# Performance work log

Measured on AMD Instinct MI355X. Metric: run time of the kernel, lower is better.

Reference implementation:

```python
import jax, jax.numpy as jnp
import numpy as np

NUM_HEADS = 8
CH_PER_HEAD = 40
NORM_GROUPS = 32
EPS = 1e-5


def setup_inputs() -> dict:
    key = jax.random.key(0)
    ks = jax.random.split(key, 8)
    B, C, H, W = 2, 320, 48, 48
    hid = NUM_HEADS * CH_PER_HEAD  # 320
    w_std = 0.02
    return {
        "x": jax.random.normal(ks[0], (B, C, H, W), dtype=jnp.float32),
        "gamma": jnp.ones((C,), dtype=jnp.float32),
        "beta": jnp.zeros((C,), dtype=jnp.float32),
        "Wq": jax.random.normal(ks[1], (hid, C), dtype=jnp.float32) * w_std,
        "bq": jax.random.normal(ks[2], (hid,), dtype=jnp.float32) * w_std,
        "Wk": jax.random.normal(ks[3], (hid, C), dtype=jnp.float32) * w_std,
        "bk": jax.random.normal(ks[4], (hid,), dtype=jnp.float32) * w_std,
        "Wv": jax.random.normal(ks[5], (hid, C), dtype=jnp.float32) * w_std,
        "bv": jax.random.normal(ks[6], (hid,), dtype=jnp.float32) * w_std,
        "Wo": jax.random.normal(ks[7], (C, hid), dtype=jnp.float32) * w_std,
        "bo": jnp.zeros((C,), dtype=jnp.float32),
    }


def _group_norm(x, gamma, beta):
    # x: [B, C, H, W]; GroupNorm over (C//G, H, W) per group, affine per-channel.
    B, C, H, W = x.shape
    xg = x.reshape(B, NORM_GROUPS, C // NORM_GROUPS, H, W)
    mean = xg.mean(axis=(2, 3, 4), keepdims=True)
    var = xg.var(axis=(2, 3, 4), keepdims=True)
    xn = ((xg - mean) * jax.lax.rsqrt(var + EPS)).reshape(B, C, H, W)
    return xn * gamma[None, :, None, None] + beta[None, :, None, None]


def reference(x, gamma, beta, Wq, bq, Wk, bk, Wv, bv, Wo, bo):
    B, C, H, W = x.shape
    N = H * W
    h, d = NUM_HEADS, CH_PER_HEAD
    scale = d ** (-0.25)  # applied to both q and k (net 1/sqrt(d))

    xn = _group_norm(x, gamma, beta).reshape(B, C, N)  # embedding = x_n (self-attn)

    # 1x1 Conv1d == matmul over channel dim
    q = jnp.einsum('oc,bcn->bon', Wq, xn) + bq[None, :, None]
    k = jnp.einsum('oc,bcn->bon', Wk, xn) + bk[None, :, None]
    v = jnp.einsum('oc,bcn->bon', Wv, xn) + bv[None, :, None]

    # b (h d) n -> b h d n
    q = q.reshape(B, h, d, N)
    k = k.reshape(B, h, d, N)
    v = v.reshape(B, h, d, N)

    attn = jax.nn.softmax(
        jnp.einsum('bhdi,bhdj->bhij', q * scale, k * scale), axis=-1
    )  # [B, h, N, N]
    out = jnp.einsum('bhij,bhdj->bhdi', attn, v).reshape(B, h * d, N)

    out = jnp.einsum('oc,bcn->bon', Wo, out) + bo[None, :, None]
    out = out.reshape(B, C, H, W)
    return x + out  # shapes match -> residual
```

## Files before the change

kernel.cpp:

```cpp
#include <hip/hip_runtime.h>
#include <hip/hip_bf16.h>

#define C_DIM   320
#define N_SP    2304
#define NHEADS  8
#define DHEAD   40
#define GROUPS  32
#define CPG     10
#define BATCH   2
#define DPAD    64
#define VPAD    48
#define W_ELEMS (C_DIM * C_DIM)
#define NSPLIT  4
#define TILES_PER_SPLIT 9
#define PSLOTS  41

typedef __bf16 bf16x8 __attribute__((ext_vector_type(8)));
typedef __bf16 bf16x4 __attribute__((ext_vector_type(4)));
typedef __bf16 bf16x2 __attribute__((ext_vector_type(2)));
typedef float  f32x4  __attribute__((ext_vector_type(4)));

typedef const __attribute__((address_space(1))) void* gas_ptr;
typedef __attribute__((address_space(3))) void* las_ptr;

#define MFMA16(a, b, c) __builtin_amdgcn_mfma_f32_16x16x32_bf16((a), (b), (c), 0, 0, 0)

__device__ __forceinline__ void stage8(const char* gbase, char* lbase,
                                       int chunk, int lane)
{
    const int row = chunk * 8 + (lane >> 3);
    const int cs  = (lane & 7) * 16;
    __builtin_amdgcn_global_load_lds(
        (gas_ptr)(gbase + (size_t)row * (C_DIM * 2) + (cs ^ ((row & 7) << 4))),
        (las_ptr)(lbase + chunk * 1024 + lane * 16), 16, 0, 0);
}

__device__ __forceinline__ bf16x8 lds_frag(const char* lbase, int row, int cbyte)
{
    return *(const bf16x8*)(lbase + row * 128 + (cbyte ^ ((row & 7) << 4)));
}

__global__ __launch_bounds__(256) void prep_kernel(
    const float* __restrict__ x, float* __restrict__ partials,
    const float* __restrict__ Wq, const float* __restrict__ Wk,
    const float* __restrict__ Wv, const float* __restrict__ Wo,
    __bf16* __restrict__ Wqb, __bf16* __restrict__ Wkb,
    __bf16* __restrict__ Wvb, __bf16* __restrict__ Wob,
    __bf16* __restrict__ Qt, __bf16* __restrict__ Kt, __bf16* __restrict__ Vb)
{
    if (blockIdx.x < 512) {
        const int bid = blockIdx.x;
        const int bg = bid >> 3, p = bid & 7;
        const int b = bg >> 5, g = bg & 31;
        const float* xp = x + ((size_t)b * C_DIM + g * CPG) * N_SP + p * 288;
        const int tid = threadIdx.x;

        float sum = 0.f, sq = 0.f;
        #pragma unroll
        for (int c = 0; c < CPG; ++c) {
            for (int nl = tid; nl < 288; nl += 256) {
                const float v = xp[(size_t)c * N_SP + nl];
                sum += v; sq += v * v;
            }
        }
        #pragma unroll
        for (int off = 32; off; off >>= 1) {
            sum += __shfl_xor(sum, off);
            sq  += __shfl_xor(sq, off);
        }
        __shared__ float red[2][4];
        if ((tid & 63) == 0) { red[0][tid >> 6] = sum; red[1][tid >> 6] = sq; }
        __syncthreads();
        if (tid == 0) {
            partials[2 * bid]     = red[0][0] + red[0][1] + red[0][2] + red[0][3];
            partials[2 * bid + 1] = red[1][0] + red[1][1] + red[1][2] + red[1][3];
        }
    } else if (blockIdx.x < 612) {
        const int i = ((blockIdx.x - 512) * 256 + threadIdx.x) * 4;
        f32x4 a;
        bf16x4 o;
        a = *(const f32x4*)(Wq + i);
        #pragma unroll
        for (int e = 0; e < 4; ++e) o[e] = (__bf16)a[e];
        *(bf16x4*)(Wqb + i) = o;
        a = *(const f32x4*)(Wk + i);
        #pragma unroll
        for (int e = 0; e < 4; ++e) o[e] = (__bf16)a[e];
        *(bf16x4*)(Wkb + i) = o;
        a = *(const f32x4*)(Wv + i);
        #pragma unroll
        for (int e = 0; e < 4; ++e) o[e] = (__bf16)a[e];
        *(bf16x4*)(Wvb + i) = o;
        a = *(const f32x4*)(Wo + i);
        #pragma unroll
        for (int e = 0; e < 4; ++e) o[e] = (__bf16)a[e];
        *(bf16x4*)(Wob + i) = o;
    } else {
        const int t = (blockIdx.x - 612) * 256 + threadIdx.x;
        const bf16x8 z = {};
        __bf16* q = Qt + (size_t)t * DPAD + 40;
        __bf16* k = Kt + (size_t)t * DPAD + 40;
        *(bf16x8*)(q) = z; *(bf16x8*)(q + 8) = z; *(bf16x8*)(q + 16) = z;
        *(bf16x8*)(k) = z; *(bf16x8*)(k + 8) = z; *(bf16x8*)(k + 16) = z;
        const int bh = t / N_SP;
        const int rem = t - bh * N_SP;
        const int r = rem / 288, n8 = rem - r * 288;
        bf16x8 v = z;
        if (r == 0) {
            #pragma unroll
            for (int e = 0; e < 8; ++e) v[e] = (__bf16)1.0f;
        }
        *(bf16x8*)(Vb + ((size_t)bh * VPAD + 40 + r) * N_SP + n8 * 8) = v;
    }
}

__global__ __launch_bounds__(256) void gn_apply(
    const float* __restrict__ x,
    const float* __restrict__ gamma, const float* __restrict__ beta,
    const float* __restrict__ partials, __bf16* __restrict__ xn_t)
{
    const int bid = blockIdx.x;
    const int bg = bid >> 3, p = bid & 7;
    const int b = bg >> 5, g = bg & 31;
    const int c0 = g * CPG;

    float sum = 0.f, sq = 0.f;
    #pragma unroll
    for (int i = 0; i < 8; ++i) {
        sum += partials[(bg * 8 + i) * 2];
        sq  += partials[(bg * 8 + i) * 2 + 1];
    }
    const float inv_n = 1.0f / (float)(CPG * N_SP);
    const float mean = sum * inv_n;
    const float rstd = rsqrtf(sq * inv_n - mean * mean + 1e-5f);

    float ga[CPG], be[CPG];
    #pragma unroll
    for (int c = 0; c < CPG; ++c) {
        ga[c] = gamma[c0 + c] * rstd;
        be[c] = beta[c0 + c] - mean * ga[c];
    }

    const float* xp = x + ((size_t)b * C_DIM + c0) * N_SP + p * 288;
    for (int nl = threadIdx.x; nl < 288; nl += 256) {
        const int n = p * 288 + nl;
        __bf16* dst = xn_t + ((size_t)b * N_SP + n) * C_DIM + c0;
        #pragma unroll
        for (int j = 0; j < CPG / 2; ++j) {
            const float v0 = xp[(size_t)(2 * j) * N_SP + nl]     * ga[2 * j]     + be[2 * j];
            const float v1 = xp[(size_t)(2 * j + 1) * N_SP + nl] * ga[2 * j + 1] + be[2 * j + 1];
            bf16x2 t; t[0] = (__bf16)v0; t[1] = (__bf16)v1;
            *(bf16x2*)(dst + 2 * j) = t;
        }
    }
}

__global__ __launch_bounds__(256) void gemm_qkv(
    const __bf16* __restrict__ Wqb, const __bf16* __restrict__ Wkb, const __bf16* __restrict__ Wvb,
    const float* __restrict__ bq, const float* __restrict__ bk, const float* __restrict__ bv,
    const __bf16* __restrict__ Xt,
    __bf16* __restrict__ Qt, __bf16* __restrict__ Kt, __bf16* __restrict__ Vb)
{
    __shared__ __align__(16) char Ws[2][64 * 128];
    __shared__ __align__(16) char Xs[2][64 * 128];

    const int z = blockIdx.z;
    const int b = z / 3;
    const int which = z - 3 * b;
    const __bf16* W   = (which == 0) ? Wqb : (which == 1) ? Wkb : Wvb;
    const float* bias = (which == 0) ? bq : (which == 1) ? bk : bv;
    const float scale = (which == 0) ? 0.15811388300841897f
                      : (which == 1) ? 0.22811243f : 1.0f;

    const int n0 = blockIdx.x * 64, o0 = blockIdx.y * 64;
    const int tid = threadIdx.x, wave = tid >> 6, lane = tid & 63;
    const int lr = lane & 15, lk = lane >> 4;
    const int wm = wave >> 1, wn = wave & 1;

    const char* Wg = (const char*)(W + (size_t)o0 * C_DIM);
    const char* Xg = (const char*)(Xt + ((size_t)b * N_SP + n0) * C_DIM);

    auto stage = [&](int bufi, int s) {
        const int kb = s * 128;
        #pragma unroll
        for (int i = 0; i < 4; ++i) {
            const int c = wave * 4 + i;
            if (c < 8) stage8(Wg + kb, Ws[bufi], c, lane);
            else       stage8(Xg + kb, Xs[bufi], c - 8, lane);
        }
    };

    f32x4 acc[2][2] = {};

    stage(0, 0);
    __syncthreads();

    for (int s = 0; s < 5; ++s) {
        const int bufi = s & 1;
        if (s + 1 < 5) stage(bufi ^ 1, s + 1);

        const char* ws = Ws[bufi];
        const char* xs = Xs[bufi];
        __builtin_amdgcn_s_setprio(1);
        #pragma unroll
        for (int ksub = 0; ksub < 2; ++ksub) {
            const int cb = ksub * 64 + lk * 16;
            const bf16x8 a0 = lds_frag(ws, wm * 32 + lr,      cb);
            const bf16x8 a1 = lds_frag(ws, wm * 32 + 16 + lr, cb);
            const bf16x8 b0 = lds_frag(xs, wn * 32 + lr,      cb);
            const bf16x8 b1 = lds_frag(xs, wn * 32 + 16 + lr, cb);
            acc[0][0] = MFMA16(a0, b0, acc[0][0]);
            acc[0][1] = MFMA16(a0, b1, acc[0][1]);
            acc[1][0] = MFMA16(a1, b0, acc[1][0]);
            acc[1][1] = MFMA16(a1, b1, acc[1][1]);
        }
        __builtin_amdgcn_s_setprio(0);
        __syncthreads();
    }

    #pragma unroll
    for (int am = 0; am < 2; ++am) {
        #pragma unroll
        for (int rp = 0; rp < 2; ++rp) {
            const int o = o0 + wm * 32 + am * 16 + 4 * lk + 2 * rp;
            const int h = o / DHEAD, d = o - h * DHEAD;
            const int bh = b * NHEADS + h;
            const float b0_ = bias[o], b1_ = bias[o + 1];
            #pragma unroll
            for (int bn = 0; bn < 2; ++bn) {
                const int n = n0 + wn * 32 + bn * 16 + lr;
                const float v0 = (acc[am][bn][2 * rp]     + b0_) * scale;
                const float v1 = (acc[am][bn][2 * rp + 1] + b1_) * scale;
                if (which < 2) {
                    __bf16* dst = ((which == 0) ? Qt : Kt)
                                + ((size_t)bh * N_SP + n) * DPAD + d;
                    bf16x2 t; t[0] = (__bf16)v0; t[1] = (__bf16)v1;
                    *(bf16x2*)dst = t;
                } else {
                    Vb[((size_t)bh * VPAD + d)     * N_SP + n] = (__bf16)v0;
                    Vb[((size_t)bh * VPAD + d + 1) * N_SP + n] = (__bf16)v1;
                }
            }
        }
    }
}

__global__ __launch_bounds__(256) void gemm_out32(
    const __bf16* __restrict__ Wob, const float* __restrict__ bo,
    const __bf16* __restrict__ att_t,
    float* __restrict__ Y, const float* __restrict__ resid)
{
    __shared__ __align__(16) char Ws[2][32 * 128];
    __shared__ __align__(16) char Xs[2][64 * 128];

    const int b = blockIdx.z;
    const int n0 = blockIdx.x * 64, o0 = blockIdx.y * 32;
    const int tid = threadIdx.x, wave = tid >> 6, lane = tid & 63;
    const int lr = lane & 15, lk = lane >> 4;
    const int wn = wave;

    const char* Wg = (const char*)(Wob + (size_t)o0 * C_DIM);
    const char* Xg = (const char*)(att_t + ((size_t)b * N_SP + n0) * C_DIM);

    auto stage = [&](int bufi, int s) {
        const int kb = s * 128;
        #pragma unroll
        for (int i = 0; i < 3; ++i) {
            const int c = wave * 3 + i;
            if (c < 4) stage8(Wg + kb, Ws[bufi], c, lane);
            else       stage8(Xg + kb, Xs[bufi], c - 4, lane);
        }
    };

    f32x4 acc[2] = {};

    stage(0, 0);
    __syncthreads();

    for (int s = 0; s < 5; ++s) {
        const int bufi = s & 1;
        if (s + 1 < 5) stage(bufi ^ 1, s + 1);

        const char* ws = Ws[bufi];
        const char* xs = Xs[bufi];
        __builtin_amdgcn_s_setprio(1);
        #pragma unroll
        for (int ksub = 0; ksub < 2; ++ksub) {
            const int cb = ksub * 64 + lk * 16;
            const bf16x8 a0 = lds_frag(ws, lr,      cb);
            const bf16x8 a1 = lds_frag(ws, 16 + lr, cb);
            const bf16x8 b0 = lds_frag(xs, wn * 16 + lr, cb);
            acc[0] = MFMA16(a0, b0, acc[0]);
            acc[1] = MFMA16(a1, b0, acc[1]);
        }
        __builtin_amdgcn_s_setprio(0);
        __syncthreads();
    }

    const int n = n0 + wn * 16 + lr;
    #pragma unroll
    for (int am = 0; am < 2; ++am) {
        #pragma unroll
        for (int r = 0; r < 4; ++r) {
            const int o = o0 + am * 16 + 4 * lk + r;
            const size_t idx = ((size_t)b * C_DIM + o) * N_SP + n;
            Y[idx] = acc[am][r] + bo[o] + resid[idx];
        }
    }
}

__global__ __launch_bounds__(256) void attn_mfma(
    const __bf16* __restrict__ Qt,
    const __bf16* __restrict__ Kt,
    const __bf16* __restrict__ Vb,
    __bf16* __restrict__ part)
{
    __shared__ __align__(16) __bf16 Ks[2][64 * DPAD];
    __shared__ __align__(16) __bf16 Vs[2][VPAD * 64];
    __shared__ __align__(16) __bf16 Ps[4][16 * 64];

    const int flat = blockIdx.x;
    const int bh = ((flat & 7) << 1) | ((flat >> 3) & 1);
    const int s  = (flat >> 4) & 3;
    const int qx = flat >> 6;
    const int tid = threadIdx.x, wave = tid >> 6, lane = tid & 63;
    const int lr = lane & 15, lk = lane >> 4;
    const int swz = (lr & 7) << 4;
    const int i0 = (qx * 4 + wave) * 16;

    const char* Kg = (const char*)(Kt + (size_t)bh * N_SP * DPAD);
    const char* Vg = (const char*)(Vb + (size_t)bh * VPAD * N_SP);

    const __bf16* Qp = Qt + ((size_t)bh * N_SP + i0 + lr) * DPAD + lk * 8;
    const bf16x8 qb0 = *(const bf16x8*)(Qp);
    const bf16x8 qb1 = *(const bf16x8*)(Qp + 32);

    f32x4 O[3] = {};

    auto stage = [&](int bufi, int t) {
        const int j0 = t * 64;
        #pragma unroll
        for (int i2 = 0; i2 < 2; ++i2) {
            const int chunk = wave * 2 + i2;
            const int L = chunk * 1024 + lane * 16;
            const int src = L ^ (((L >> 7) & 7) << 4);
            __builtin_amdgcn_global_load_lds(
                (gas_ptr)(Kg + (size_t)j0 * 128 + src),
                (las_ptr)((char*)Ks[bufi] + chunk * 1024),
                16, 0, 0);
        }
        for (int i2 = wave; i2 < 6; i2 += 4) {
            const int row = i2 * 8 + (lane >> 3);
            const int csw = ((lane & 7) << 4) ^ ((row & 7) << 4);
            __builtin_amdgcn_global_load_lds(
                (gas_ptr)(Vg + ((size_t)row * N_SP + j0) * 2 + csw),
                (las_ptr)((char*)Vs[bufi] + i2 * 1024),
                16, 0, 0);
        }
    };

    const int t0 = s * TILES_PER_SPLIT;
    const int t1 = t0 + TILES_PER_SPLIT;

    stage(0, t0);

    for (int t = t0; t < t1; ++t) {
        const int bufi = (t - t0) & 1;
        if (t + 1 < t1) {
            stage(bufi ^ 1, t + 1);
            if (wave < 2) asm volatile("s_waitcnt vmcnt(4)" ::: "memory");
            else          asm volatile("s_waitcnt vmcnt(3)" ::: "memory");
        } else {
            asm volatile("s_waitcnt vmcnt(0)" ::: "memory");
        }
        __builtin_amdgcn_s_barrier();

        const char* ks = (const char*)Ks[bufi];
        const char* vs = (const char*)Vs[bufi];
        char* ps = (char*)Ps[wave];

        f32x4 S[4];
        __builtin_amdgcn_s_setprio(1);
        #pragma unroll
        for (int kt = 0; kt < 4; ++kt) {
            const int rowb = (kt * 16 + lr) * 128;
            const bf16x8 k0 = *(const bf16x8*)(ks + rowb + ((lk * 16) ^ swz));
            const bf16x8 k1 = *(const bf16x8*)(ks + rowb + ((64 + lk * 16) ^ swz));
            f32x4 zz = {};
            zz = MFMA16(k0, qb0, zz);
            S[kt] = MFMA16(k1, qb1, zz);
        }
        __builtin_amdgcn_s_setprio(0);

        #pragma unroll
        for (int kt = 0; kt < 4; ++kt) {
            bf16x4 w;
            #pragma unroll
            for (int r = 0; r < 4; ++r)
                w[r] = (__bf16)exp2f(S[kt][r]);
            *(bf16x4*)(ps + lr * 128 + ((kt * 32 + lk * 8) ^ swz)) = w;
        }

        __builtin_amdgcn_s_setprio(1);
        #pragma unroll
        for (int hh = 0; hh < 2; ++hh) {
            const bf16x8 pb = *(const bf16x8*)(ps + lr * 128 + ((hh * 64 + lk * 16) ^ swz));
            #pragma unroll
            for (int dt = 0; dt < 3; ++dt) {
                const bf16x8 va = *(const bf16x8*)(vs + (dt * 16 + lr) * 128 + ((hh * 64 + lk * 16) ^ swz));
                O[dt] = MFMA16(va, pb, O[dt]);
            }
        }
        __builtin_amdgcn_s_setprio(0);

        __builtin_amdgcn_s_barrier();
    }

    __bf16* pq = part + ((size_t)(s * 16 + bh) * PSLOTS) * N_SP + (i0 + lr);
    #pragma unroll
    for (int dt = 0; dt < 3; ++dt) {
        #pragma unroll
        for (int r = 0; r < 4; ++r) {
            const int d = dt * 16 + 4 * lk + r;
            if (d < 40) pq[(size_t)d * N_SP] = (__bf16)O[dt][r];
        }
    }
    if (lk == 2) pq[(size_t)40 * N_SP] = (__bf16)O[2][0];
}

__global__ __launch_bounds__(256) void attn_combine(
    const __bf16* __restrict__ part, __bf16* __restrict__ att_t)
{
    const int q = blockIdx.x * 256 + threadIdx.x;
    const int bh = blockIdx.y, b = bh >> 3, h = bh & 7;

    const __bf16* p[NSPLIT];
    float l = 0.f;
    #pragma unroll
    for (int s = 0; s < NSPLIT; ++s) {
        p[s] = part + ((size_t)(s * 16 + bh) * PSLOTS) * N_SP + q;
        l += (float)p[s][(size_t)40 * N_SP];
    }
    const float inv = 1.0f / l;

    __bf16* op = att_t + ((size_t)b * N_SP + q) * C_DIM + h * DHEAD;
    #pragma unroll
    for (int d2 = 0; d2 < DHEAD / 2; ++d2) {
        float a0 = 0.f, a1 = 0.f;
        #pragma unroll
        for (int s = 0; s < NSPLIT; ++s) {
            a0 += (float)p[s][(size_t)(2 * d2) * N_SP];
            a1 += (float)p[s][(size_t)(2 * d2 + 1) * N_SP];
        }
        bf16x2 t;
        t[0] = (__bf16)(a0 * inv);
        t[1] = (__bf16)(a1 * inv);
        *(bf16x2*)(op + 2 * d2) = t;
    }
}

extern "C" void kernel_launch(void* const* d_in, const int* in_sizes, int n_in,
                              void* d_out, int out_size, void* d_ws, size_t ws_size,
                              hipStream_t stream) {
    const float* x     = (const float*)d_in[0];
    const float* gamma = (const float*)d_in[1];
    const float* beta  = (const float*)d_in[2];
    const float* Wq    = (const float*)d_in[3];
    const float* bq    = (const float*)d_in[4];
    const float* Wk    = (const float*)d_in[5];
    const float* bk    = (const float*)d_in[6];
    const float* Wv    = (const float*)d_in[7];
    const float* bv    = (const float*)d_in[8];
    const float* Wo    = (const float*)d_in[9];
    const float* bo    = (const float*)d_in[10];

    float* out = (float*)d_out;

    const size_t S_NC  = (size_t)BATCH * N_SP * C_DIM;
    const size_t S_QK  = (size_t)BATCH * NHEADS * N_SP * DPAD;
    const size_t S_V   = (size_t)BATCH * NHEADS * VPAD * N_SP;

    __bf16* xn_t  = (__bf16*)d_ws;
    __bf16* Qt    = xn_t + S_NC;
    __bf16* Kt    = Qt + S_QK;
    __bf16* Vb    = Kt + S_QK;
    __bf16* att_t = Vb + S_V;
    __bf16* Wqb   = att_t + S_NC;
    __bf16* Wkb   = Wqb + W_ELEMS;
    __bf16* Wvb   = Wkb + W_ELEMS;
    __bf16* Wob   = Wvb + W_ELEMS;
    float* partials = (float*)(Wob + W_ELEMS);
    __bf16* part    = (__bf16*)(partials + 1024);

    prep_kernel<<<756, 256, 0, stream>>>(
        x, partials, Wq, Wk, Wv, Wo, Wqb, Wkb, Wvb, Wob, Qt, Kt, Vb);

    gn_apply<<<512, 256, 0, stream>>>(x, gamma, beta, partials, xn_t);

    gemm_qkv<<<dim3(N_SP / 64, C_DIM / 64, 3 * BATCH), 256, 0, stream>>>(
        Wqb, Wkb, Wvb, bq, bk, bv, xn_t, Qt, Kt, Vb);

    attn_mfma<<<dim3(36 * 16 * NSPLIT), 256, 0, stream>>>(Qt, Kt, Vb, part);

    attn_combine<<<dim3(N_SP / 256, BATCH * NHEADS), 256, 0, stream>>>(part, att_t);

    gemm_out32<<<dim3(N_SP / 64, C_DIM / 32, BATCH), 256, 0, stream>>>(
        Wob, bo, att_t, out, x);
}
```

Baseline: 81.16 us.

## Process two query tiles per wave in attention to reuse K/V fragments

```diff
diff --git a/kernel.cpp b/kernel.cpp
--- a/kernel.cpp
+++ b/kernel.cpp
@@ -309,7 +309,7 @@
     }
 }
 
-__global__ __launch_bounds__(256) void attn_mfma(
+__global__ __launch_bounds__(256, 4) void attn_mfma(
     const __bf16* __restrict__ Qt,
     const __bf16* __restrict__ Kt,
     const __bf16* __restrict__ Vb,
@@ -326,16 +326,20 @@
     const int tid = threadIdx.x, wave = tid >> 6, lane = tid & 63;
     const int lr = lane & 15, lk = lane >> 4;
     const int swz = (lr & 7) << 4;
-    const int i0 = (qx * 4 + wave) * 16;
+    const int i0 = (qx * 4 + wave) * 32;
 
     const char* Kg = (const char*)(Kt + (size_t)bh * N_SP * DPAD);
     const char* Vg = (const char*)(Vb + (size_t)bh * VPAD * N_SP);
 
-    const __bf16* Qp = Qt + ((size_t)bh * N_SP + i0 + lr) * DPAD + lk * 8;
-    const bf16x8 qb0 = *(const bf16x8*)(Qp);
-    const bf16x8 qb1 = *(const bf16x8*)(Qp + 32);
-
-    f32x4 O[3] = {};
+    bf16x8 qb[2][2];
+    #pragma unroll
+    for (int qh = 0; qh < 2; ++qh) {
+        const __bf16* Qp = Qt + ((size_t)bh * N_SP + i0 + qh * 16 + lr) * DPAD + lk * 8;
+        qb[qh][0] = *(const bf16x8*)(Qp);
+        qb[qh][1] = *(const bf16x8*)(Qp + 32);
+    }
+
+    f32x4 O[2][3] = {};
 
     auto stage = [&](int bufi, int t) {
         const int j0 = t * 64;
@@ -379,53 +383,67 @@
         const char* vs = (const char*)Vs[bufi];
         char* ps = (char*)Ps[wave];
 
-        f32x4 S[4];
+        f32x4 S[2][4];
         __builtin_amdgcn_s_setprio(1);
         #pragma unroll
         for (int kt = 0; kt < 4; ++kt) {
             const int rowb = (kt * 16 + lr) * 128;
             const bf16x8 k0 = *(const bf16x8*)(ks + rowb + ((lk * 16) ^ swz));
             const bf16x8 k1 = *(const bf16x8*)(ks + rowb + ((64 + lk * 16) ^ swz));
-            f32x4 zz = {};
-            zz = MFMA16(k0, qb0, zz);
-            S[kt] = MFMA16(k1, qb1, zz);
+            #pragma unroll
+            for (int qh = 0; qh < 2; ++qh) {
+                f32x4 zz = {};
+                zz = MFMA16(k0, qb[qh][0], zz);
+                S[qh][kt] = MFMA16(k1, qb[qh][1], zz);
+            }
         }
         __builtin_amdgcn_s_setprio(0);
 
-        #pragma unroll
-        for (int kt = 0; kt < 4; ++kt) {
-            bf16x4 w;
-            #pragma unroll
-            for (int r = 0; r < 4; ++r)
-                w[r] = (__bf16)exp2f(S[kt][r]);
-            *(bf16x4*)(ps + lr * 128 + ((kt * 32 + lk * 8) ^ swz)) = w;
-        }
-
-        __builtin_amdgcn_s_setprio(1);
-        #pragma unroll
-        for (int hh = 0; hh < 2; ++hh) {
-            const bf16x8 pb = *(const bf16x8*)(ps + lr * 128 + ((hh * 64 + lk * 16) ^ swz));
-            #pragma unroll
-            for (int dt = 0; dt < 3; ++dt) {
-                const bf16x8 va = *(const bf16x8*)(vs + (dt * 16 + lr) * 128 + ((hh * 64 + lk * 16) ^ swz));
-                O[dt] = MFMA16(va, pb, O[dt]);
+        bf16x8 va[2][3];
+        #pragma unroll
+        for (int hh = 0; hh < 2; ++hh)
+            #pragma unroll
+            for (int dt = 0; dt < 3; ++dt)
+                va[hh][dt] = *(const bf16x8*)(vs + (dt * 16 + lr) * 128
+                                              + ((hh * 64 + lk * 16) ^ swz));
+
+        #pragma unroll
+        for (int qh = 0; qh < 2; ++qh) {
+            #pragma unroll
+            for (int kt = 0; kt < 4; ++kt) {
+                bf16x4 w;
+                #pragma unroll
+                for (int r = 0; r < 4; ++r)
+                    w[r] = (__bf16)exp2f(S[qh][kt][r]);
+                *(bf16x4*)(ps + lr * 128 + ((kt * 32 + lk * 8) ^ swz)) = w;
             }
-        }
-        __builtin_amdgcn_s_setprio(0);
+            __builtin_amdgcn_s_setprio(1);
+            #pragma unroll
+            for (int hh = 0; hh < 2; ++hh) {
+                const bf16x8 pb = *(const bf16x8*)(ps + lr * 128 + ((hh * 64 + lk * 16) ^ swz));
+                #pragma unroll
+                for (int dt = 0; dt < 3; ++dt)
+                    O[qh][dt] = MFMA16(va[hh][dt], pb, O[qh][dt]);
+            }
+            __builtin_amdgcn_s_setprio(0);
+        }
 
         __builtin_amdgcn_s_barrier();
     }
 
-    __bf16* pq = part + ((size_t)(s * 16 + bh) * PSLOTS) * N_SP + (i0 + lr);
-    #pragma unroll
-    for (int dt = 0; dt < 3; ++dt) {
-        #pragma unroll
-        for (int r = 0; r < 4; ++r) {
-            const int d = dt * 16 + 4 * lk + r;
-            if (d < 40) pq[(size_t)d * N_SP] = (__bf16)O[dt][r];
-        }
-    }
-    if (lk == 2) pq[(size_t)40 * N_SP] = (__bf16)O[2][0];
+    #pragma unroll
+    for (int qh = 0; qh < 2; ++qh) {
+        __bf16* pq = part + ((size_t)(s * 16 + bh) * PSLOTS) * N_SP + (i0 + qh * 16 + lr);
+        #pragma unroll
+        for (int dt = 0; dt < 3; ++dt) {
+            #pragma unroll
+            for (int r = 0; r < 4; ++r) {
+                const int d = dt * 16 + 4 * lk + r;
+                if (d < 40) pq[(size_t)d * N_SP] = (__bf16)O[qh][dt][r];
+            }
+        }
+        if (lk == 2) pq[(size_t)40 * N_SP] = (__bf16)O[qh][2][0];
+    }
 }
 
 __global__ __launch_bounds__(256) void attn_combine(
@@ -500,7 +518,7 @@
     gemm_qkv<<<dim3(N_SP / 64, C_DIM / 64, 3 * BATCH), 256, 0, stream>>>(
         Wqb, Wkb, Wvb, bq, bk, bv, xn_t, Qt, Kt, Vb);
 
-    attn_mfma<<<dim3(36 * 16 * NSPLIT), 256, 0, stream>>>(Qt, Kt, Vb, part);
+    attn_mfma<<<dim3(18 * 16 * NSPLIT), 256, 0, stream>>>(Qt, Kt, Vb, part);
 
     attn_combine<<<dim3(N_SP / 256, BATCH * NHEADS), 256, 0, stream>>>(part, att_t);
 
```

Measured after the change: 78.72 us. 3.0% less time.
